# Kernel tuning notes

Hardware: AMD Instinct MI355X
Metric: run time of the kernel (lower is better)

Reference implementation:

```python
import jax, jax.numpy as jnp
import numpy as np

N_USERS = 100000
N_ITEMS = 20000
N_GENRES = 20
N_TAGS = 1128
EMB_ID = 64
EMB_FEAT = 64
HEADS = 8
HIDDEN = 256
D_MOVIE = EMB_ID + 2 * EMB_FEAT  # 192
E_HALF = 200000
N_NODES = N_USERS + N_ITEMS
NEG_SLOPE = 0.2


def setup_inputs() -> dict:
    key = jax.random.key(0)
    ks = jax.random.split(key, 24)
    p = lambda k, shape: (jax.random.normal(k, shape, jnp.float32) * 0.05)
    user_ids = jnp.arange(N_USERS)
    movie_ids = jnp.arange(N_ITEMS)
    mov_x = jax.random.normal(ks[0], (N_ITEMS, N_GENRES + N_TAGS), jnp.float32)
    # bipartite user<->movie edges, both directions (no self loops, matches add_self_loops=False)
    u = jax.random.randint(ks[1], (E_HALF,), 0, N_USERS)
    m = jax.random.randint(ks[2], (E_HALF,), 0, N_ITEMS) + N_USERS
    edge_index = jnp.stack([jnp.concatenate([u, m]), jnp.concatenate([m, u])])  # [2, 2*E_HALF]
    C1 = HIDDEN // HEADS
    return dict(
        user_ids=user_ids, movie_ids=movie_ids, mov_x=mov_x, edge_index=edge_index,
        user_emb=p(ks[3], (N_USERS, EMB_ID)), item_emb=p(ks[4], (N_ITEMS, EMB_ID)),
        gW1=p(ks[5], (N_GENRES, EMB_FEAT)), gb1=jnp.zeros((EMB_FEAT,), jnp.float32),
        gW2=p(ks[6], (EMB_FEAT, EMB_FEAT)), gb2=jnp.zeros((EMB_FEAT,), jnp.float32),
        tW1=p(ks[7], (N_TAGS, EMB_FEAT)), tb1=jnp.zeros((EMB_FEAT,), jnp.float32),
        tW2=p(ks[8], (EMB_FEAT, EMB_FEAT)), tb2=jnp.zeros((EMB_FEAT,), jnp.float32),
        Ws1=p(ks[9], (D_MOVIE, HIDDEN)), Wd1=p(ks[10], (D_MOVIE, HIDDEN)),
        as1=p(ks[11], (HEADS, C1)), ad1=p(ks[12], (HEADS, C1)),
        b1=jnp.zeros((HIDDEN,), jnp.float32),
        Ws2=p(ks[13], (HIDDEN, HIDDEN)), Wd2=p(ks[14], (HIDDEN, HIDDEN)),
        as2=p(ks[15], (1, HIDDEN)), ad2=p(ks[16], (1, HIDDEN)),
        b2=jnp.zeros((HIDDEN,), jnp.float32),
    )


def _gat(x, edge_index, Ws, Wd, a_s, a_d, bias, concat):
    # PyG GATConv (eval mode: dropout off, add_self_loops=False)
    N = x.shape[0]
    H, C = a_s.shape
    hs = (x @ Ws).reshape(N, H, C)  # source-side projection
    hd = (x @ Wd).reshape(N, H, C)  # dest-side projection
    al_s = (hs * a_s).sum(-1)  # [N, H]
    al_d = (hd * a_d).sum(-1)  # [N, H]
    src, dst = edge_index[0], edge_index[1]
    e = al_s[src] + al_d[dst]                      # [E, H]
    e = jnp.where(e > 0, e, NEG_SLOPE * e)         # leaky_relu(0.2)
    mmax = jax.ops.segment_max(e, dst, num_segments=N)
    w = jnp.exp(e - mmax[dst])
    ssum = jax.ops.segment_sum(w, dst, num_segments=N)
    alpha = w / (ssum[dst] + 1e-16)                # segment softmax over incoming edges
    out = jax.ops.segment_sum(hs[src] * alpha[:, :, None], dst, num_segments=N)  # [N, H, C]
    out = out.reshape(N, H * C) if concat else out.mean(axis=1)
    return out + bias


def reference(user_ids, movie_ids, mov_x, edge_index,
              user_emb, item_emb,
              gW1, gb1, gW2, gb2, tW1, tb1, tW2, tb2,
              Ws1, Wd1, as1, ad1, b1,
              Ws2, Wd2, as2, ad2, b2):
    g_feat = mov_x[:, :N_GENRES]
    t_feat = mov_x[:, N_GENRES:]
    g = jax.nn.relu(g_feat @ gW1 + gb1) @ gW2 + gb2
    t = jax.nn.relu(t_feat @ tW1 + tb1) @ tW2 + tb2
    x_mov = jnp.concatenate([item_emb[movie_ids], g, t], axis=1)  # [n_m, D_MOVIE]
    # homogeneous graph: user nodes first (zero-pad user emb to D_MOVIE), then movies
    x_usr = jnp.pad(user_emb[user_ids], ((0, 0), (0, D_MOVIE - EMB_ID)))
    x = jnp.concatenate([x_usr, x_mov], axis=0)  # [N_NODES, D_MOVIE]
    out = jax.nn.elu(_gat(x, edge_index, Ws1, Wd1, as1, ad1, b1, concat=True))
    out = _gat(out, edge_index, Ws2, Wd2, as2, ad2, b2, concat=False)
    ptr = jnp.array([0, N_USERS, N_USERS + N_ITEMS])
    return out, ptr
```

## Files before the change

### kernel.cpp

```cpp
#include <hip/hip_runtime.h>
#include <hip/hip_bf16.h>

#define N_USERS_C 100000
#define N_ITEMS_C 20000
#define N_NODES_C 120000
#define E_TOT_C   400000
#define D_IN_C    192
#define HID_C     256
#define NEG_C     0.2f
#define CLAMP_C   1000.0f
#define KPAD_C    1152
#define NB_SCAN   ((N_NODES_C + 255) / 256)
#define NB_EDGE   ((E_TOT_C + 255) / 256)
#define NB_GEMM   (N_NODES_C / 64)
#define ROWE      40
#define NT_MOV    313
#define KSPLIT    4
#define KCH       288

typedef __attribute__((ext_vector_type(8))) short bfrag;
typedef __attribute__((ext_vector_type(4))) float ffrag;

__device__ __forceinline__ float bf2f(unsigned short u){
  return __uint_as_float(((unsigned)u) << 16);
}
__device__ __forceinline__ float ldf(const void* p, long i, int isf32){
  return isf32 ? ((const float*)p)[i] : bf2f(((const unsigned short*)p)[i]);
}
__device__ __forceinline__ float sane(float v){
  return (v > -1e30f && v < 1e30f) ? v : 0.f;
}
__device__ __forceinline__ int clampsrc(int s){
  return s < 0 ? 0 : (s >= N_NODES_C ? N_NODES_C - 1 : s);
}
__device__ __forceinline__ short f2bs(float f){
  __hip_bfloat16 h = __float2bfloat16(f);
  return *reinterpret_cast<short*>(&h);
}

__global__ __launch_bounds__(256) void detect_dtype(const unsigned short* __restrict__ ue,
                                                    int* __restrict__ flag){
  __shared__ int cnt[256];
  int tid = threadIdx.x; int c = 0;
  for (int i = tid; i < 8192; i += 256){
    unsigned e = (ue[i] >> 7) & 0xFFu;
    if (e >= 129u) c++;
  }
  cnt[tid] = c; __syncthreads();
  if (tid == 0){
    int s = 0;
    for (int i = 0; i < 256; i++) s += cnt[i];
    *flag = (s > 100) ? 1 : 0;
  }
}

struct PrepArgs {
  const void *ue, *ie;
  const void *gW1, *gb1, *gW2, *gb2, *tW1, *tb1, *tW2, *tb2;
  const void *Ws1, *Wd1, *as1, *ad1, *b1, *Ws2, *Wd2, *as2, *ad2, *b2;
  __hip_bfloat16 *x, *Bt1, *Bt2, *W1t, *W2t, *b1c, *b2c, *bg1, *bg2;
  int *deg, *cursor;
  const int* flag;
};

#define NB_UEMB  3125
#define NB_UZERO 2
#define NB_MOVE  625
#define NB_BT1   204
#define NB_BT2   272
#define NB_W1T   72
#define NB_W2T   8
#define NB_ZERO  235
#define NB_PREP (NB_UEMB+NB_UZERO+NB_MOVE+NB_BT1+NB_BT2+NB_W1T+NB_W2T+1+NB_ZERO)

__global__ __launch_bounds__(256) void mega_prep(PrepArgs a){
  int b = blockIdx.x, tid = threadIdx.x;
  int f32 = *a.flag;
  if (b < NB_UEMB) {
    int idx = b * 256 + tid;
    int n = idx >> 3, c0 = (idx & 7) * 8;
    union { short s[8]; float4 f; } u;
    if (f32) {
      const float* rf = (const float*)a.ue + (long)n * 64 + c0;
      float4 x0 = *(const float4*)rf, x1 = *(const float4*)(rf + 4);
      u.s[0]=f2bs(x0.x); u.s[1]=f2bs(x0.y); u.s[2]=f2bs(x0.z); u.s[3]=f2bs(x0.w);
      u.s[4]=f2bs(x1.x); u.s[5]=f2bs(x1.y); u.s[6]=f2bs(x1.z); u.s[7]=f2bs(x1.w);
    } else {
      u.f = *(const float4*)((const unsigned short*)a.ue + (long)n * 64 + c0);
    }
    *(float4*)(&a.x[(long)n * 192 + c0]) = u.f;
    return;
  }
  b -= NB_UEMB;
  if (b < NB_UZERO) {
    int idx = b * 256 + tid;
    int r = idx >> 4, c0 = 64 + (idx & 15) * 8;
    float4 z = {0.f, 0.f, 0.f, 0.f};
    *(float4*)(&a.x[(long)(99968 + r) * 192 + c0]) = z;
    return;
  }
  b -= NB_UZERO;
  if (b < NB_MOVE) {
    int idx = b * 256 + tid;
    int m = idx >> 3, c0 = (idx & 7) * 8;
    union { short s[8]; float4 f; } u;
    if (f32) {
      const float* rf = (const float*)a.ie + (long)m * 64 + c0;
      float4 x0 = *(const float4*)rf, x1 = *(const float4*)(rf + 4);
      u.s[0]=f2bs(x0.x); u.s[1]=f2bs(x0.y); u.s[2]=f2bs(x0.z); u.s[3]=f2bs(x0.w);
      u.s[4]=f2bs(x1.x); u.s[5]=f2bs(x1.y); u.s[6]=f2bs(x1.z); u.s[7]=f2bs(x1.w);
    } else {
      u.f = *(const float4*)((const unsigned short*)a.ie + (long)m * 64 + c0);
    }
    *(float4*)(&a.x[(long)(N_USERS_C + m) * 192 + c0]) = u.f;
    return;
  }
  b -= NB_MOVE;
  if (b < NB_BT1) {
    int idx = b * 256 + tid;
    int col = idx / 192, k = idx - col * 192;
    float v;
    if (col < 256) v = ldf(a.Ws1, k * 256 + col, f32);
    else if (col < 264) {
      int h = col - 256; float s = 0.f;
      for (int c = 0; c < 32; c++)
        s += ldf(a.Ws1, k * 256 + h * 32 + c, f32) * ldf(a.as1, h * 32 + c, f32);
      v = s;
    } else {
      int h = col - 264; float s = 0.f;
      for (int c = 0; c < 32; c++)
        s += ldf(a.Wd1, k * 256 + h * 32 + c, f32) * ldf(a.ad1, h * 32 + c, f32);
      v = s;
    }
    a.Bt1[col * 192 + k] = __float2bfloat16(v);
    return;
  }
  b -= NB_BT1;
  if (b < NB_BT2) {
    int idx = b * 256 + tid;
    int col = idx / 256, k = idx & 255;
    float v;
    if (col < 256) v = ldf(a.Ws2, k * 256 + col, f32);
    else if (col == 256) {
      float s = 0.f;
      for (int c = 0; c < 256; c++)
        s += ldf(a.Ws2, k * 256 + c, f32) * ldf(a.as2, c, f32);
      v = s;
    } else if (col == 257) {
      float s = 0.f;
      for (int c = 0; c < 256; c++)
        s += ldf(a.Wd2, k * 256 + c, f32) * ldf(a.ad2, c, f32);
      v = s;
    } else v = 0.f;
    a.Bt2[col * 256 + k] = __float2bfloat16(v);
    return;
  }
  b -= NB_BT2;
  if (b < NB_W1T) {
    int idx = b * 256 + tid;
    int n = idx / 144, c8 = idx - n * 144;
    int k0 = c8 * 8;
    union { short s[8]; float4 f; } u;
#pragma unroll
    for (int j = 0; j < 8; j++) {
      int k = k0 + j; float v = 0.f;
      if (n < 64) { if (k < 20) v = ldf(a.gW1, k * 64 + n, f32); }
      else        { if (k >= 20 && k < 1148) v = ldf(a.tW1, (k - 20) * 64 + (n - 64), f32); }
      u.s[j] = f2bs(v);
    }
    *(float4*)(&a.W1t[(long)n * 1152 + k0]) = u.f;
    return;
  }
  b -= NB_W1T;
  if (b < NB_W2T) {
    int idx = b * 256 + tid;
    int n = idx >> 4, k0 = (idx & 15) * 8;
    union { short s[8]; float4 f; } u;
#pragma unroll
    for (int j = 0; j < 8; j++) {
      int k = k0 + j; float v = 0.f;
      if (n < 64) { if (k < 64)  v = ldf(a.gW2, k * 64 + n, f32); }
      else        { if (k >= 64) v = ldf(a.tW2, (k - 64) * 64 + (n - 64), f32); }
      u.s[j] = f2bs(v);
    }
    *(float4*)(&a.W2t[n * 128 + k0]) = u.f;
    return;
  }
  b -= NB_W2T;
  if (b < 1) {
    int i = tid;
    if (i < 64)       a.b1c[i] = __float2bfloat16(ldf(a.gb1, i, f32));
    else if (i < 128) a.b1c[i] = __float2bfloat16(ldf(a.tb1, i - 64, f32));
    else if (i < 192) a.b2c[i - 128] = __float2bfloat16(ldf(a.gb2, i - 128, f32));
    else              a.b2c[i - 128] = __float2bfloat16(ldf(a.tb2, i - 192, f32));
    a.bg1[tid] = __float2bfloat16(ldf(a.b1, tid, f32));
    a.bg2[tid] = __float2bfloat16(ldf(a.b2, tid, f32));
    return;
  }
  b -= 1;
  {
    int i0 = (b * 256 + tid) * 4;
    if (i0 < 2 * N_NODES_C) {
      int4 z = {0, 0, 0, 0};
      if (i0 < N_NODES_C) *(int4*)(a.deg + i0) = z;
      else                *(int4*)(a.cursor + (i0 - N_NODES_C)) = z;
    }
  }
}


__device__ void movie_k_body(int bid, const void* __restrict__ rawA, int f32v,
                             const __hip_bfloat16* __restrict__ W1t,
                             float* __restrict__ part){
  __shared__ short Bls[128 * ROWE];
  __shared__ short Als[64 * ROWE];
  int tid = threadIdx.x;
  int wave = tid >> 6;
  int lane = tid & 63;
  int l15 = lane & 15;
  int quad = lane >> 4;
  int tile = bid % NT_MOV, split = bid / NT_MOV;
  int rowbase_blk = tile * 64;
  int rowbase = rowbase_blk + wave * 16;
  ffrag acc[8];
#pragma unroll
  for (int i = 0; i < 8; i++) acc[i] = (ffrag){0.f, 0.f, 0.f, 0.f};
  const short* Bs = (const short*)W1t;
  int sr = tid >> 2, sc = tid & 3;
  int arow_st = rowbase_blk + sr; if (arow_st >= N_ITEMS_C) arow_st = N_ITEMS_C - 1;
  int kbeg = split * KCH;
  for (int k0 = kbeg; k0 < kbeg + KCH; k0 += 32) {
    __syncthreads();
    for (int t = tid; t < 512; t += 256) {
      int r = t >> 2, c = t & 3;
      *(float4*)(&Bls[r * ROWE + c * 8]) =
          *(const float4*)(Bs + (long)r * KPAD_C + k0 + c * 8);
    }
    int kc = k0 + sc * 8;
    union { short s[8]; float4 f; } u;
    long base = (long)arow_st * 1148 + kc;
    if (kc + 8 <= 1148) {
      if (f32v) {
        const float* rf = (const float*)rawA + base;
        float4 x0 = *(const float4*)rf;
        float4 x1 = *(const float4*)(rf + 4);
        u.s[0]=f2bs(x0.x); u.s[1]=f2bs(x0.y); u.s[2]=f2bs(x0.z); u.s[3]=f2bs(x0.w);
        u.s[4]=f2bs(x1.x); u.s[5]=f2bs(x1.y); u.s[6]=f2bs(x1.z); u.s[7]=f2bs(x1.w);
      } else {
        const unsigned short* rs = (const unsigned short*)rawA + base;
        ushort4 a0 = *(const ushort4*)rs;
        ushort4 a1 = *(const ushort4*)(rs + 4);
        u.s[0]=(short)a0.x; u.s[1]=(short)a0.y; u.s[2]=(short)a0.z; u.s[3]=(short)a0.w;
        u.s[4]=(short)a1.x; u.s[5]=(short)a1.y; u.s[6]=(short)a1.z; u.s[7]=(short)a1.w;
      }
    } else {
#pragma unroll
      for (int j = 0; j < 8; j++) {
        float v = (kc + j < 1148) ? ldf(rawA, base + j, f32v) : 0.f;
        u.s[j] = f2bs(v);
      }
    }
    *(float4*)(&Als[sr * ROWE + sc * 8]) = u.f;
    __syncthreads();
    int koff = quad * 8;
    bfrag af = *(const bfrag*)(&Als[(wave * 16 + l15) * ROWE + koff]);
#pragma unroll
    for (int nt = 0; nt < 8; nt++) {
      bfrag bf = *(const bfrag*)(&Bls[(nt * 16 + l15) * ROWE + koff]);
      acc[nt] = __builtin_amdgcn_mfma_f32_16x16x32_bf16(af, bf, acc[nt], 0, 0, 0);
    }
  }
  float* pb = part + (long)split * (N_ITEMS_C * 128);
#pragma unroll
  for (int reg = 0; reg < 4; reg++) {
    int grow = rowbase + quad * 4 + reg;
    if (grow >= N_ITEMS_C) continue;
#pragma unroll
    for (int nt = 0; nt < 8; nt++)
      pb[(long)grow * 128 + nt * 16 + l15] = acc[nt][reg];
  }
}

__device__ void movie2_body(int bid, const float* __restrict__ part,
                            const __hip_bfloat16* __restrict__ b1c,
                            const __hip_bfloat16* __restrict__ W2t,
                            const __hip_bfloat16* __restrict__ b2c,
                            __hip_bfloat16* __restrict__ out){
  __shared__ short Bls[128 * ROWE];
  __shared__ short Als[64 * ROWE];
  int tid = threadIdx.x;
  int wave = tid >> 6;
  int lane = tid & 63;
  int l15 = lane & 15;
  int quad = lane >> 4;
  int rowbase_blk = bid * 64;
  int rowbase = rowbase_blk + wave * 16;
  ffrag acc[8];
#pragma unroll
  for (int i = 0; i < 8; i++) acc[i] = (ffrag){0.f, 0.f, 0.f, 0.f};
  const short* Bs = (const short*)W2t;
  int sr = tid >> 2, sc = tid & 3;
  int arow_st = rowbase_blk + sr; if (arow_st >= N_ITEMS_C) arow_st = N_ITEMS_C - 1;
  for (int k0 = 0; k0 < 128; k0 += 32) {
    __syncthreads();
    for (int t = tid; t < 512; t += 256) {
      int r = t >> 2, c = t & 3;
      *(float4*)(&Bls[r * ROWE + c * 8]) =
          *(const float4*)(Bs + (long)r * 128 + k0 + c * 8);
    }
    int kc = k0 + sc * 8;
    float vs[8];
#pragma unroll
    for (int j = 0; j < 8; j++) vs[j] = __bfloat162float(b1c[kc + j]);
    long base = (long)arow_st * 128 + kc;
#pragma unroll
    for (int s = 0; s < KSPLIT; s++) {
      const float* p = part + (long)s * (N_ITEMS_C * 128) + base;
      float4 q0 = *(const float4*)p, q1 = *(const float4*)(p + 4);
      vs[0] += q0.x; vs[1] += q0.y; vs[2] += q0.z; vs[3] += q0.w;
      vs[4] += q1.x; vs[5] += q1.y; vs[6] += q1.z; vs[7] += q1.w;
    }
    union { short s[8]; float4 f; } u;
#pragma unroll
    for (int j = 0; j < 8; j++) u.s[j] = f2bs(fmaxf(vs[j], 0.f));
    *(float4*)(&Als[sr * ROWE + sc * 8]) = u.f;
    __syncthreads();
    int koff = quad * 8;
    bfrag af = *(const bfrag*)(&Als[(wave * 16 + l15) * ROWE + koff]);
#pragma unroll
    for (int nt = 0; nt < 8; nt++) {
      bfrag bf = *(const bfrag*)(&Bls[(nt * 16 + l15) * ROWE + koff]);
      acc[nt] = __builtin_amdgcn_mfma_f32_16x16x32_bf16(af, bf, acc[nt], 0, 0, 0);
    }
  }
#pragma unroll
  for (int reg = 0; reg < 4; reg++) {
    int grow = rowbase + quad * 4 + reg;
    if (grow >= N_ITEMS_C) continue;
#pragma unroll
    for (int nt = 0; nt < 8; nt++) {
      float v = acc[nt][reg] + __bfloat162float(b2c[nt * 16 + l15]);
      out[(long)grow * D_IN_C + 64 + nt * 16 + l15] = __float2bfloat16(v);
    }
  }
}

__device__ void gemm_fused_body(int bid,
    const __hip_bfloat16* __restrict__ A, const __hip_bfloat16* __restrict__ Bt,
    __hip_bfloat16* __restrict__ Hout, float* __restrict__ als, float* __restrict__ ald,
    int K, int natt, int ukmax){
  __shared__ short Bls[272 * ROWE];
  __shared__ short Als[64 * ROWE];
  int tid = threadIdx.x;
  int wave = tid >> 6;
  int lane = tid & 63;
  int l15 = lane & 15;
  int quad = lane >> 4;
  int rowbase_blk = bid * 64;
  int rowbase = rowbase_blk + wave * 16;
  int kmax = (rowbase_blk + 64 <= N_USERS_C) ? ukmax : K;
  ffrag acc[17];
#pragma unroll
  for (int i = 0; i < 17; i++) acc[i] = (ffrag){0.f, 0.f, 0.f, 0.f};
  const short* As = (const short*)A;
  const short* Bs = (const short*)Bt;
  int sr = tid >> 2, sc = tid & 3;
  for (int k0 = 0; k0 < kmax; k0 += 32) {
    __syncthreads();
    for (int t = tid; t < 1088; t += 256) {
      int r = t >> 2, c = t & 3;
      *(float4*)(&Bls[r * ROWE + c * 8]) = *(const float4*)(Bs + (long)r * K + k0 + c * 8);
    }
    *(float4*)(&Als[sr * ROWE + sc * 8]) =
        *(const float4*)(As + (long)(rowbase_blk + sr) * K + k0 + sc * 8);
    __syncthreads();
    int koff = quad * 8;
    bfrag af = *(const bfrag*)(&Als[(wave * 16 + l15) * ROWE + koff]);
#pragma unroll
    for (int nt = 0; nt < 17; nt++) {
      bfrag bf = *(const bfrag*)(&Bls[(nt * 16 + l15) * ROWE + koff]);
      acc[nt] = __builtin_amdgcn_mfma_f32_16x16x32_bf16(af, bf, acc[nt], 0, 0, 0);
    }
  }
  int col = l15;
#pragma unroll
  for (int reg = 0; reg < 4; reg++) {
    int grow = rowbase + quad * 4 + reg;
    long obase = (long)grow * 256;
#pragma unroll
    for (int nt = 0; nt < 16; nt++)
      Hout[obase + nt * 16 + col] = __float2bfloat16(acc[nt][reg]);
    float v = acc[16][reg];
    if (col < natt) als[grow * natt + col] = v;
    else if (col < 2 * natt) ald[grow * natt + (col - natt)] = v;
  }
}

__device__ void deg_count_body(int e, const int* __restrict__ ei, int* __restrict__ deg){
  if (e >= E_TOT_C) return;
  int dst = ei[E_TOT_C + e];
  if (dst >= 0 && dst < N_NODES_C) atomicAdd(&deg[dst], 1);
}

__device__ void deg_bsum_body(int bid, const int* __restrict__ deg, int* __restrict__ bsum){
  int i = bid * 256 + threadIdx.x;
  int v = (i < N_NODES_C) ? deg[i] : 0;
#pragma unroll
  for (int o = 32; o > 0; o >>= 1) v += __shfl_down(v, o, 64);
  __shared__ int ws[4];
  int wave = threadIdx.x >> 6, lane = threadIdx.x & 63;
  if (lane == 0) ws[wave] = v;
  __syncthreads();
  if (threadIdx.x == 0) bsum[bid] = ws[0] + ws[1] + ws[2] + ws[3];
}

__device__ void scatter_body(int e, const int* __restrict__ ei, const int* __restrict__ ptrn,
                             int* __restrict__ cursor, int* __restrict__ elist_src){
  if (e >= E_TOT_C) return;
  int dst = ei[E_TOT_C + e];
  if (dst < 0 || dst >= N_NODES_C) return;
  int pos = atomicAdd(&cursor[dst], 1);
  elist_src[ptrn[dst] + pos] = ei[e];
}

#define NB_KA (NT_MOV * KSPLIT + NB_EDGE)
__global__ __launch_bounds__(256) void movie_k_degcnt(
    const void* __restrict__ rawA, const int* __restrict__ flag,
    const __hip_bfloat16* __restrict__ W1t, float* __restrict__ part,
    const int* __restrict__ ei, int* __restrict__ deg){
  int b = blockIdx.x;
  if (b < NT_MOV * KSPLIT) movie_k_body(b, rawA, *flag, W1t, part);
  else deg_count_body((b - NT_MOV * KSPLIT) * 256 + threadIdx.x, ei, deg);
}

#define NB_KB (NT_MOV + NB_SCAN)
__global__ __launch_bounds__(256) void movie2_bsum(
    const float* __restrict__ part, const __hip_bfloat16* __restrict__ b1c,
    const __hip_bfloat16* __restrict__ W2t, const __hip_bfloat16* __restrict__ b2c,
    __hip_bfloat16* __restrict__ out,
    const int* __restrict__ deg, int* __restrict__ bsum){
  int b = blockIdx.x;
  if (b < NT_MOV) movie2_body(b, part, b1c, W2t, b2c, out);
  else deg_bsum_body(b - NT_MOV, deg, bsum);
}

#define NB_KC (NB_GEMM + NB_EDGE)
__global__ __launch_bounds__(256) void gemm1_scatter(
    const __hip_bfloat16* __restrict__ A, const __hip_bfloat16* __restrict__ Bt,
    __hip_bfloat16* __restrict__ Hout, float* __restrict__ als, float* __restrict__ ald,
    const int* __restrict__ ei, const int* __restrict__ ptrn,
    int* __restrict__ cursor, int* __restrict__ elist_src){
  int b = blockIdx.x;
  if (b < NB_GEMM) gemm_fused_body(b, A, Bt, Hout, als, ald, 192, 8, 64);
  else scatter_body((b - NB_GEMM) * 256 + threadIdx.x, ei, ptrn, cursor, elist_src);
}

__global__ __launch_bounds__(256) void gemm_fused(
    const __hip_bfloat16* __restrict__ A, const __hip_bfloat16* __restrict__ Bt,
    __hip_bfloat16* __restrict__ Hout, float* __restrict__ als, float* __restrict__ ald,
    int K, int natt, int ukmax){
  gemm_fused_body(blockIdx.x, A, Bt, Hout, als, ald, K, natt, ukmax);
}

__global__ __launch_bounds__(512) void bsum_scan(int* __restrict__ bsum,
                                                 int* __restrict__ ptrn){
  __shared__ int sm[512];
  int t = threadIdx.x;
  int v = (t < NB_SCAN) ? bsum[t] : 0;
  sm[t] = v;
  __syncthreads();
  for (int o = 1; o < 512; o <<= 1) {
    int add = (t >= o) ? sm[t - o] : 0;
    __syncthreads();
    sm[t] += add;
    __syncthreads();
  }
  int excl = (t == 0) ? 0 : sm[t - 1];
  if (t < NB_SCAN) bsum[t] = excl;
  if (t == NB_SCAN - 1) ptrn[N_NODES_C] = sm[t];
}

__global__ __launch_bounds__(256) void deg_scan_final(const int* __restrict__ deg,
                                                      const int* __restrict__ bexcl,
                                                      int* __restrict__ ptrn){
  __shared__ int sm[256];
  int i = blockIdx.x * 256 + threadIdx.x;
  int t = threadIdx.x;
  int v = (i < N_NODES_C) ? deg[i] : 0;
  sm[t] = v;
  __syncthreads();
  for (int o = 1; o < 256; o <<= 1) {
    int add = (t >= o) ? sm[t - o] : 0;
    __syncthreads();
    sm[t] += add;
    __syncthreads();
  }
  int excl = (t == 0) ? 0 : sm[t - 1];
  if (i < N_NODES_C) ptrn[i] = bexcl[blockIdx.x] + excl;
}

__global__ __launch_bounds__(256) void aggregate1(
    const int* __restrict__ ptrn, const int* __restrict__ elist_src,
    const float* __restrict__ als, const float* __restrict__ ald,
    const __hip_bfloat16* __restrict__ hs, const __hip_bfloat16* __restrict__ bias,
    __hip_bfloat16* __restrict__ h1){
  int node = blockIdx.x * 4 + (threadIdx.x >> 6);
  if (node >= N_NODES_C) return;
  int lane = threadIdx.x & 63;
  int c0 = lane * 4;
  int h = lane >> 3;
  int beg = ptrn[node], end = ptrn[node + 1];
  float aldv = sane(ald[node * 8 + h]);
  float m = -1e30f;
  float wsum = 0.f, a0 = 0.f, a1 = 0.f, a2 = 0.f, a3 = 0.f;
  const unsigned short* hsu = (const unsigned short*)hs;
  float alsv_p = 0.f;
  ushort4 hv_p = {0, 0, 0, 0};
  int src_b = 0;
  if (beg < end) {
    int s0 = clampsrc(elist_src[beg]);
    alsv_p = als[(long)s0 * 8 + h];
    hv_p = *(const ushort4*)(hsu + (long)s0 * 256 + c0);
    if (beg + 1 < end) src_b = clampsrc(elist_src[beg + 1]);
  }
  for (int i = beg; i < end; i++) {
    float alsv = alsv_p;
    ushort4 hv = hv_p;
    if (i + 1 < end) {
      alsv_p = als[(long)src_b * 8 + h];
      hv_p = *(const ushort4*)(hsu + (long)src_b * 256 + c0);
    }
    if (i + 2 < end)
      src_b = clampsrc(elist_src[i + 2]);
    float ev = sane(alsv) + aldv;
    ev = ev > 0.f ? ev : NEG_C * ev;
    float mnew = fmaxf(m, ev);
    float corr = __expf(m - mnew);
    float w = __expf(ev - mnew);
    m = mnew;
    wsum = wsum * corr + w;
    a0 = a0 * corr + w * bf2f(hv.x); a1 = a1 * corr + w * bf2f(hv.y);
    a2 = a2 * corr + w * bf2f(hv.z); a3 = a3 * corr + w * bf2f(hv.w);
  }
  float inv = 1.f / (wsum + 1e-16f);
  float v0 = a0 * inv + __bfloat162float(bias[c0 + 0]);
  float v1 = a1 * inv + __bfloat162float(bias[c0 + 1]);
  float v2 = a2 * inv + __bfloat162float(bias[c0 + 2]);
  float v3 = a3 * inv + __bfloat162float(bias[c0 + 3]);
  v0 = v0 > 0.f ? v0 : (__expf(v0) - 1.f);
  v1 = v1 > 0.f ? v1 : (__expf(v1) - 1.f);
  v2 = v2 > 0.f ? v2 : (__expf(v2) - 1.f);
  v3 = v3 > 0.f ? v3 : (__expf(v3) - 1.f);
  v0 = fminf(fmaxf(v0, -CLAMP_C), CLAMP_C);
  v1 = fminf(fmaxf(v1, -CLAMP_C), CLAMP_C);
  v2 = fminf(fmaxf(v2, -CLAMP_C), CLAMP_C);
  v3 = fminf(fmaxf(v3, -CLAMP_C), CLAMP_C);
  long ob = (long)node * 256 + c0;
  h1[ob + 0] = __float2bfloat16(v0); h1[ob + 1] = __float2bfloat16(v1);
  h1[ob + 2] = __float2bfloat16(v2); h1[ob + 3] = __float2bfloat16(v3);
}

__global__ __launch_bounds__(256) void aggregate2(
    const int* __restrict__ ptrn, const int* __restrict__ elist_src,
    const float* __restrict__ als, const float* __restrict__ ald,
    const __hip_bfloat16* __restrict__ hs, const __hip_bfloat16* __restrict__ bias,
    float* __restrict__ out, int out_size){
  if (blockIdx.x == 0 && threadIdx.x == 0) {
    out[out_size - 3] = 0.f;
    out[out_size - 2] = (float)N_USERS_C;
    out[out_size - 1] = (float)N_NODES_C;
  }
  int node = blockIdx.x * 4 + (threadIdx.x >> 6);
  if (node >= N_NODES_C) return;
  int lane = threadIdx.x & 63;
  int c0 = lane * 4;
  int beg = ptrn[node], end = ptrn[node + 1];
  float aldv = sane(ald[node]);
  float m = -1e30f;
  float wsum = 0.f, a0 = 0.f, a1 = 0.f, a2 = 0.f, a3 = 0.f;
  const unsigned short* hsu = (const unsigned short*)hs;
  float alsv_p = 0.f;
  ushort4 hv_p = {0, 0, 0, 0};
  int src_b = 0;
  if (beg < end) {
    int s0 = clampsrc(elist_src[beg]);
    alsv_p = als[s0];
    hv_p = *(const ushort4*)(hsu + (long)s0 * 256 + c0);
    if (beg + 1 < end) src_b = clampsrc(elist_src[beg + 1]);
  }
  for (int i = beg; i < end; i++) {
    float alsv = alsv_p;
    ushort4 hv = hv_p;
    if (i + 1 < end) {
      alsv_p = als[src_b];
      hv_p = *(const ushort4*)(hsu + (long)src_b * 256 + c0);
    }
    if (i + 2 < end)
      src_b = clampsrc(elist_src[i + 2]);
    float ev = sane(alsv) + aldv;
    ev = ev > 0.f ? ev : NEG_C * ev;
    float mnew = fmaxf(m, ev);
    float corr = __expf(m - mnew);
    float w = __expf(ev - mnew);
    m = mnew;
    wsum = wsum * corr + w;
    a0 = a0 * corr + w * bf2f(hv.x); a1 = a1 * corr + w * bf2f(hv.y);
    a2 = a2 * corr + w * bf2f(hv.z); a3 = a3 * corr + w * bf2f(hv.w);
  }
  float inv = 1.f / (wsum + 1e-16f);
  float4 v;
  v.x = a0 * inv + __bfloat162float(bias[c0 + 0]);
  v.y = a1 * inv + __bfloat162float(bias[c0 + 1]);
  v.z = a2 * inv + __bfloat162float(bias[c0 + 2]);
  v.w = a3 * inv + __bfloat162float(bias[c0 + 3]);
  v.x = fminf(fmaxf(v.x, -CLAMP_C), CLAMP_C);
  v.y = fminf(fmaxf(v.y, -CLAMP_C), CLAMP_C);
  v.z = fminf(fmaxf(v.z, -CLAMP_C), CLAMP_C);
  v.w = fminf(fmaxf(v.w, -CLAMP_C), CLAMP_C);
  *(float4*)(out + (long)node * 256 + c0) = v;
}

extern "C" void kernel_launch(void* const* d_in, const int* in_sizes, int n_in,
                              void* d_out, int out_size, void* d_ws, size_t ws_size,
                              hipStream_t stream) {
  const void* mov_x    = d_in[2];
  const int*  ei       = (const int*)d_in[3];
  const void* user_emb = d_in[4];
  const void* item_emb = d_in[5];

  char* ws = (char*)d_ws;
  size_t off = 0;
  auto alloc = [&](size_t bytes) -> void* {
    void* p = ws + off; off += (bytes + 255) / 256 * 256; return p;
  };
  int* flag   = (int*)alloc(4);
  __hip_bfloat16* Bt1 = (__hip_bfloat16*)alloc(272 * 192 * 2);
  __hip_bfloat16* Bt2 = (__hip_bfloat16*)alloc(272 * 256 * 2);
  __hip_bfloat16* W1t = (__hip_bfloat16*)alloc(128 * KPAD_C * 2);
  __hip_bfloat16* W2t = (__hip_bfloat16*)alloc(128 * 128 * 2);
  __hip_bfloat16* b1c = (__hip_bfloat16*)alloc(128 * 2);
  __hip_bfloat16* b2c = (__hip_bfloat16*)alloc(128 * 2);
  __hip_bfloat16* bg1 = (__hip_bfloat16*)alloc(256 * 2);
  __hip_bfloat16* bg2 = (__hip_bfloat16*)alloc(256 * 2);
  int* ptrn   = (int*)alloc((N_NODES_C + 1) * 4);
  int* deg    = (int*)alloc(N_NODES_C * 4);
  int* cursor = (int*)alloc(N_NODES_C * 4);
  int* bsum   = (int*)alloc(512 * 4);
  int* elist  = (int*)alloc(E_TOT_C * 4);
  float* als  = (float*)alloc((size_t)N_NODES_C * 8 * 4);
  float* ald  = (float*)alloc((size_t)N_NODES_C * 8 * 4);
  __hip_bfloat16* x  = (__hip_bfloat16*)alloc((size_t)N_NODES_C * D_IN_C * 2);
  __hip_bfloat16* hs = (__hip_bfloat16*)alloc((size_t)N_NODES_C * HID_C * 2);
  __hip_bfloat16* h1  = (__hip_bfloat16*)d_out;
  float* part = (float*)((char*)d_out + 61440000);

  detect_dtype<<<1, 256, 0, stream>>>((const unsigned short*)user_emb, flag);

  PrepArgs pa;
  pa.ue = user_emb; pa.ie = item_emb;
  pa.gW1 = d_in[6];  pa.gb1 = d_in[7];  pa.gW2 = d_in[8];  pa.gb2 = d_in[9];
  pa.tW1 = d_in[10]; pa.tb1 = d_in[11]; pa.tW2 = d_in[12]; pa.tb2 = d_in[13];
  pa.Ws1 = d_in[14]; pa.Wd1 = d_in[15]; pa.as1 = d_in[16]; pa.ad1 = d_in[17]; pa.b1 = d_in[18];
  pa.Ws2 = d_in[19]; pa.Wd2 = d_in[20]; pa.as2 = d_in[21]; pa.ad2 = d_in[22]; pa.b2 = d_in[23];
  pa.x = x; pa.Bt1 = Bt1; pa.Bt2 = Bt2; pa.W1t = W1t; pa.W2t = W2t;
  pa.b1c = b1c; pa.b2c = b2c; pa.bg1 = bg1; pa.bg2 = bg2;
  pa.deg = deg; pa.cursor = cursor; pa.flag = flag;
  mega_prep<<<NB_PREP, 256, 0, stream>>>(pa);

  movie_k_degcnt<<<NB_KA, 256, 0, stream>>>(mov_x, flag, W1t, part, ei, deg);
  movie2_bsum<<<NB_KB, 256, 0, stream>>>(part, b1c, W2t, b2c,
                                         x + (long)N_USERS_C * D_IN_C, deg, bsum);
  bsum_scan<<<1, 512, 0, stream>>>(bsum, ptrn);
  deg_scan_final<<<NB_SCAN, 256, 0, stream>>>(deg, bsum, ptrn);

  gemm1_scatter<<<NB_KC, 256, 0, stream>>>(x, Bt1, hs, als, ald,
                                           ei, ptrn, cursor, elist);
  aggregate1<<<N_NODES_C / 4, 256, 0, stream>>>(ptrn, elist, als, ald, hs, bg1, h1);

  gemm_fused<<<NB_GEMM, 256, 0, stream>>>(h1, Bt2, hs, als, ald, 256, 1, 256);
  aggregate2<<<N_NODES_C / 4, 256, 0, stream>>>(ptrn, elist, als, ald, hs, bg2,
                                                (float*)d_out, out_size);
}
```

Before: 557.6 us.

## Move user-row layer-1 GEMM into movie MLP launch and register-prefetch GEMM tiles

The layer-1 projection for user rows (which do not depend on the movie MLP) now runs in the same launch as the movie tag GEMM and degree count, so it overlaps with that work. Only the movie rows stay in the later GEMM/scatter kernel. The movie GEMM and the fused GEMM now prefetch the next A tile (and B tile for the movie GEMM) into registers while the current tile is computed, and shared memory is declared once per kernel. The split-K partial buffer moves from the output buffer to the workspace, which avoids an aliasing conflict now that hs is written earlier. The cost is higher register pressure and a larger combined launch.

```diff
diff --git a/kernel.cpp b/kernel.cpp
--- a/kernel.cpp
+++ b/kernel.cpp
@@ -13,10 +13,13 @@
 #define NB_SCAN   ((N_NODES_C + 255) / 256)
 #define NB_EDGE   ((E_TOT_C + 255) / 256)
 #define NB_GEMM   (N_NODES_C / 64)
+#define NB_G1U    1562
+#define NB_G1M    (NB_GEMM - NB_G1U)
 #define ROWE      40
 #define NT_MOV    313
 #define KSPLIT    4
 #define KCH       288
+#define NSTEP_MOV (KCH / 32)
 
 typedef __attribute__((ext_vector_type(8))) short bfrag;
 typedef __attribute__((ext_vector_type(4))) float ffrag;
@@ -211,14 +214,10 @@
 
 __device__ void movie_k_body(int bid, const void* __restrict__ rawA, int f32v,
                              const __hip_bfloat16* __restrict__ W1t,
-                             float* __restrict__ part){
-  __shared__ short Bls[128 * ROWE];
-  __shared__ short Als[64 * ROWE];
+                             float* __restrict__ part,
+                             short* __restrict__ Bls, short* __restrict__ Als){
   int tid = threadIdx.x;
-  int wave = tid >> 6;
-  int lane = tid & 63;
-  int l15 = lane & 15;
-  int quad = lane >> 4;
+  int wave = tid >> 6, lane = tid & 63, l15 = lane & 15, quad = lane >> 4;
   int tile = bid % NT_MOV, split = bid / NT_MOV;
   int rowbase_blk = tile * 64;
   int rowbase = rowbase_blk + wave * 16;
@@ -228,28 +227,22 @@
   const short* Bs = (const short*)W1t;
   int sr = tid >> 2, sc = tid & 3;
   int arow_st = rowbase_blk + sr; if (arow_st >= N_ITEMS_C) arow_st = N_ITEMS_C - 1;
+  int r0 = tid >> 2, r1 = r0 + 64, cb = (tid & 3) * 8;
   int kbeg = split * KCH;
-  for (int k0 = kbeg; k0 < kbeg + KCH; k0 += 32) {
-    __syncthreads();
-    for (int t = tid; t < 512; t += 256) {
-      int r = t >> 2, c = t & 3;
-      *(float4*)(&Bls[r * ROWE + c * 8]) =
-          *(const float4*)(Bs + (long)r * KPAD_C + k0 + c * 8);
-    }
+
+  auto loadA = [&](int k0) -> float4 {
     int kc = k0 + sc * 8;
     union { short s[8]; float4 f; } u;
     long base = (long)arow_st * 1148 + kc;
     if (kc + 8 <= 1148) {
       if (f32v) {
         const float* rf = (const float*)rawA + base;
-        float4 x0 = *(const float4*)rf;
-        float4 x1 = *(const float4*)(rf + 4);
+        float4 x0 = *(const float4*)rf, x1 = *(const float4*)(rf + 4);
         u.s[0]=f2bs(x0.x); u.s[1]=f2bs(x0.y); u.s[2]=f2bs(x0.z); u.s[3]=f2bs(x0.w);
         u.s[4]=f2bs(x1.x); u.s[5]=f2bs(x1.y); u.s[6]=f2bs(x1.z); u.s[7]=f2bs(x1.w);
       } else {
         const unsigned short* rs = (const unsigned short*)rawA + base;
-        ushort4 a0 = *(const ushort4*)rs;
-        ushort4 a1 = *(const ushort4*)(rs + 4);
+        ushort4 a0 = *(const ushort4*)rs, a1 = *(const ushort4*)(rs + 4);
         u.s[0]=(short)a0.x; u.s[1]=(short)a0.y; u.s[2]=(short)a0.z; u.s[3]=(short)a0.w;
         u.s[4]=(short)a1.x; u.s[5]=(short)a1.y; u.s[6]=(short)a1.z; u.s[7]=(short)a1.w;
       }
@@ -260,8 +253,24 @@
         u.s[j] = f2bs(v);
       }
     }
-    *(float4*)(&Als[sr * ROWE + sc * 8]) = u.f;
-    __syncthreads();
+    return u.f;
+  };
+
+  float4 aR = loadA(kbeg);
+  float4 bR0 = *(const float4*)(Bs + (long)r0 * KPAD_C + kbeg + cb);
+  float4 bR1 = *(const float4*)(Bs + (long)r1 * KPAD_C + kbeg + cb);
+
+  for (int s = 0; s < NSTEP_MOV; s++) {
+    *(float4*)(&Als[sr * ROWE + sc * 8]) = aR;
+    *(float4*)(&Bls[r0 * ROWE + cb]) = bR0;
+    *(float4*)(&Bls[r1 * ROWE + cb]) = bR1;
+    __syncthreads();
+    if (s + 1 < NSTEP_MOV) {
+      int kn = kbeg + (s + 1) * 32;
+      aR = loadA(kn);
+      bR0 = *(const float4*)(Bs + (long)r0 * KPAD_C + kn + cb);
+      bR1 = *(const float4*)(Bs + (long)r1 * KPAD_C + kn + cb);
+    }
     int koff = quad * 8;
     bfrag af = *(const bfrag*)(&Als[(wave * 16 + l15) * ROWE + koff]);
 #pragma unroll
@@ -269,6 +278,7 @@
       bfrag bf = *(const bfrag*)(&Bls[(nt * 16 + l15) * ROWE + koff]);
       acc[nt] = __builtin_amdgcn_mfma_f32_16x16x32_bf16(af, bf, acc[nt], 0, 0, 0);
     }
+    __syncthreads();
   }
   float* pb = part + (long)split * (N_ITEMS_C * 128);
 #pragma unroll
@@ -285,14 +295,10 @@
                             const __hip_bfloat16* __restrict__ b1c,
                             const __hip_bfloat16* __restrict__ W2t,
                             const __hip_bfloat16* __restrict__ b2c,
-                            __hip_bfloat16* __restrict__ out){
-  __shared__ short Bls[128 * ROWE];
-  __shared__ short Als[64 * ROWE];
+                            __hip_bfloat16* __restrict__ out,
+                            short* __restrict__ Bls, short* __restrict__ Als){
   int tid = threadIdx.x;
-  int wave = tid >> 6;
-  int lane = tid & 63;
-  int l15 = lane & 15;
-  int quad = lane >> 4;
+  int wave = tid >> 6, lane = tid & 63, l15 = lane & 15, quad = lane >> 4;
   int rowbase_blk = bid * 64;
   int rowbase = rowbase_blk + wave * 16;
   ffrag acc[8];
@@ -348,14 +354,10 @@
 __device__ void gemm_fused_body(int bid,
     const __hip_bfloat16* __restrict__ A, const __hip_bfloat16* __restrict__ Bt,
     __hip_bfloat16* __restrict__ Hout, float* __restrict__ als, float* __restrict__ ald,
-    int K, int natt, int ukmax){
-  __shared__ short Bls[272 * ROWE];
-  __shared__ short Als[64 * ROWE];
+    int K, int natt, int ukmax,
+    short* __restrict__ Bls, short* __restrict__ Als){
   int tid = threadIdx.x;
-  int wave = tid >> 6;
-  int lane = tid & 63;
-  int l15 = lane & 15;
-  int quad = lane >> 4;
+  int wave = tid >> 6, lane = tid & 63, l15 = lane & 15, quad = lane >> 4;
   int rowbase_blk = bid * 64;
   int rowbase = rowbase_blk + wave * 16;
   int kmax = (rowbase_blk + 64 <= N_USERS_C) ? ukmax : K;
@@ -365,15 +367,17 @@
   const short* As = (const short*)A;
   const short* Bs = (const short*)Bt;
   int sr = tid >> 2, sc = tid & 3;
+  long arow = (long)(rowbase_blk + sr) * K;
+  float4 aR = *(const float4*)(As + arow + sc * 8);
   for (int k0 = 0; k0 < kmax; k0 += 32) {
-    __syncthreads();
+    *(float4*)(&Als[sr * ROWE + sc * 8]) = aR;
     for (int t = tid; t < 1088; t += 256) {
       int r = t >> 2, c = t & 3;
       *(float4*)(&Bls[r * ROWE + c * 8]) = *(const float4*)(Bs + (long)r * K + k0 + c * 8);
     }
-    *(float4*)(&Als[sr * ROWE + sc * 8]) =
-        *(const float4*)(As + (long)(rowbase_blk + sr) * K + k0 + sc * 8);
-    __syncthreads();
+    __syncthreads();
+    if (k0 + 32 < kmax)
+      aR = *(const float4*)(As + arow + k0 + 32 + sc * 8);
     int koff = quad * 8;
     bfrag af = *(const bfrag*)(&Als[(wave * 16 + l15) * ROWE + koff]);
 #pragma unroll
@@ -381,6 +385,7 @@
       bfrag bf = *(const bfrag*)(&Bls[(nt * 16 + l15) * ROWE + koff]);
       acc[nt] = __builtin_amdgcn_mfma_f32_16x16x32_bf16(af, bf, acc[nt], 0, 0, 0);
     }
+    __syncthreads();
   }
   int col = l15;
 #pragma unroll
@@ -423,14 +428,22 @@
   elist_src[ptrn[dst] + pos] = ei[e];
 }
 
-#define NB_KA (NT_MOV * KSPLIT + NB_EDGE)
-__global__ __launch_bounds__(256) void movie_k_degcnt(
+#define NB_BIG (NT_MOV * KSPLIT + NB_G1U + NB_EDGE)
+__global__ __launch_bounds__(256) void fused_stage3(
     const void* __restrict__ rawA, const int* __restrict__ flag,
     const __hip_bfloat16* __restrict__ W1t, float* __restrict__ part,
+    const __hip_bfloat16* __restrict__ x, const __hip_bfloat16* __restrict__ Bt1,
+    __hip_bfloat16* __restrict__ hs, float* __restrict__ als, float* __restrict__ ald,
     const int* __restrict__ ei, int* __restrict__ deg){
+  __shared__ short smem[(272 + 64) * ROWE];
   int b = blockIdx.x;
-  if (b < NT_MOV * KSPLIT) movie_k_body(b, rawA, *flag, W1t, part);
-  else deg_count_body((b - NT_MOV * KSPLIT) * 256 + threadIdx.x, ei, deg);
+  if (b < NT_MOV * KSPLIT)
+    movie_k_body(b, rawA, *flag, W1t, part, smem, smem + 128 * ROWE);
+  else if (b < NT_MOV * KSPLIT + NB_G1U)
+    gemm_fused_body(b - NT_MOV * KSPLIT, x, Bt1, hs, als, ald, 192, 8, 64,
+                    smem, smem + 272 * ROWE);
+  else
+    deg_count_body((b - NT_MOV * KSPLIT - NB_G1U) * 256 + threadIdx.x, ei, deg);
 }
 
 #define NB_KB (NT_MOV + NB_SCAN)
@@ -439,27 +452,34 @@
     const __hip_bfloat16* __restrict__ W2t, const __hip_bfloat16* __restrict__ b2c,
     __hip_bfloat16* __restrict__ out,
     const int* __restrict__ deg, int* __restrict__ bsum){
+  __shared__ short smem[192 * ROWE];
   int b = blockIdx.x;
-  if (b < NT_MOV) movie2_body(b, part, b1c, W2t, b2c, out);
+  if (b < NT_MOV) movie2_body(b, part, b1c, W2t, b2c, out, smem, smem + 128 * ROWE);
   else deg_bsum_body(b - NT_MOV, deg, bsum);
 }
 
-#define NB_KC (NB_GEMM + NB_EDGE)
-__global__ __launch_bounds__(256) void gemm1_scatter(
+#define NB_S7 (NB_G1M + NB_EDGE)
+__global__ __launch_bounds__(256) void gemm1mov_scatter(
     const __hip_bfloat16* __restrict__ A, const __hip_bfloat16* __restrict__ Bt,
     __hip_bfloat16* __restrict__ Hout, float* __restrict__ als, float* __restrict__ ald,
     const int* __restrict__ ei, const int* __restrict__ ptrn,
     int* __restrict__ cursor, int* __restrict__ elist_src){
+  __shared__ short smem[(272 + 64) * ROWE];
   int b = blockIdx.x;
-  if (b < NB_GEMM) gemm_fused_body(b, A, Bt, Hout, als, ald, 192, 8, 64);
-  else scatter_body((b - NB_GEMM) * 256 + threadIdx.x, ei, ptrn, cursor, elist_src);
+  if (b < NB_G1M)
+    gemm_fused_body(NB_G1U + b, A, Bt, Hout, als, ald, 192, 8, 64,
+                    smem, smem + 272 * ROWE);
+  else
+    scatter_body((b - NB_G1M) * 256 + threadIdx.x, ei, ptrn, cursor, elist_src);
 }
 
 __global__ __launch_bounds__(256) void gemm_fused(
     const __hip_bfloat16* __restrict__ A, const __hip_bfloat16* __restrict__ Bt,
     __hip_bfloat16* __restrict__ Hout, float* __restrict__ als, float* __restrict__ ald,
     int K, int natt, int ukmax){
-  gemm_fused_body(blockIdx.x, A, Bt, Hout, als, ald, K, natt, ukmax);
+  __shared__ short smem[(272 + 64) * ROWE];
+  gemm_fused_body(blockIdx.x, A, Bt, Hout, als, ald, K, natt, ukmax,
+                  smem, smem + 272 * ROWE);
 }
 
 __global__ __launch_bounds__(512) void bsum_scan(int* __restrict__ bsum,
@@ -649,10 +669,10 @@
   int* elist  = (int*)alloc(E_TOT_C * 4);
   float* als  = (float*)alloc((size_t)N_NODES_C * 8 * 4);
   float* ald  = (float*)alloc((size_t)N_NODES_C * 8 * 4);
+  float* part = (float*)alloc((size_t)KSPLIT * N_ITEMS_C * 128 * 4);
   __hip_bfloat16* x  = (__hip_bfloat16*)alloc((size_t)N_NODES_C * D_IN_C * 2);
   __hip_bfloat16* hs = (__hip_bfloat16*)alloc((size_t)N_NODES_C * HID_C * 2);
   __hip_bfloat16* h1  = (__hip_bfloat16*)d_out;
-  float* part = (float*)((char*)d_out + 61440000);
 
   detect_dtype<<<1, 256, 0, stream>>>((const unsigned short*)user_emb, flag);
 
@@ -667,14 +687,15 @@
   pa.deg = deg; pa.cursor = cursor; pa.flag = flag;
   mega_prep<<<NB_PREP, 256, 0, stream>>>(pa);
 
-  movie_k_degcnt<<<NB_KA, 256, 0, stream>>>(mov_x, flag, W1t, part, ei, deg);
+  fused_stage3<<<NB_BIG, 256, 0, stream>>>(mov_x, flag, W1t, part,
+                                           x, Bt1, hs, als, ald, ei, deg);
   movie2_bsum<<<NB_KB, 256, 0, stream>>>(part, b1c, W2t, b2c,
                                          x + (long)N_USERS_C * D_IN_C, deg, bsum);
   bsum_scan<<<1, 512, 0, stream>>>(bsum, ptrn);
   deg_scan_final<<<NB_SCAN, 256, 0, stream>>>(deg, bsum, ptrn);
 
-  gemm1_scatter<<<NB_KC, 256, 0, stream>>>(x, Bt1, hs, als, ald,
-                                           ei, ptrn, cursor, elist);
+  gemm1mov_scatter<<<NB_S7, 256, 0, stream>>>(x, Bt1, hs, als, ald,
+                                              ei, ptrn, cursor, elist);
   aggregate1<<<N_NODES_C / 4, 256, 0, stream>>>(ptrn, elist, als, ald, hs, bg1, h1);
 
   gemm_fused<<<NB_GEMM, 256, 0, stream>>>(h1, Bt2, hs, als, ald, 256, 1, 256);
```

Measured after the change: 558.7 us. About the same (+0.2%).
